# Kernel tuning notes

Measured on AMD Instinct MI355X. Metric: run time of the kernel, lower is better.

The kernel has to match this reference:

```python
import jax, jax.numpy as jnp
import numpy as np

MEM = 2048

def _linear_params(key, scale):
    kw, kb = jax.random.split(key)
    W = jax.random.uniform(kw, (MEM, MEM), jnp.float32, -scale, scale)
    b = jax.random.uniform(kb, (MEM,), jnp.float32, -scale, scale)
    return W, b

def setup_inputs() -> dict:
    key = jax.random.key(0)
    ks = jax.random.split(key, 18)
    scale = 1.0 / np.sqrt(MEM)
    inp = {
        'lc': jax.random.normal(ks[0], (1, MEM), jnp.float32),
        'lh': jax.random.normal(ks[1], (1, MEM), jnp.float32),
        'rc': jax.random.normal(ks[2], (1, MEM), jnp.float32),
        'rh': jax.random.normal(ks[3], (1, MEM), jnp.float32),
        'S': jax.random.normal(ks[4], (1, MEM), jnp.float32),
        'w': jax.random.normal(ks[5], (1, MEM), jnp.float32),
    }
    names = ['Wh', 'Us', 'ma', 'ilh', 'irh', 'lflh', 'lfrh', 'rflh', 'rfrh', 'ulh', 'urh']
    for i, n in enumerate(names):
        W, b = _linear_params(ks[6 + i], scale)
        inp[n + '_w'] = W
        inp[n + '_b'] = b
    return inp

def _lin(x, W, b):
    return x @ W.T + b

def reference(lc, lh, rc, rh, S, w,
              Wh_w, Wh_b, Us_w, Us_b, ma_w, ma_b,
              ilh_w, ilh_b, irh_w, irh_b,
              lflh_w, lflh_b, lfrh_w, lfrh_b,
              rflh_w, rflh_b, rfrh_w, rfrh_b,
              ulh_w, ulh_b, urh_w, urh_b):
    # attention scoring over the two children
    m_left = jnp.tanh(_lin(lh, Wh_w, Wh_b) + _lin(S, Us_w, Us_b)).squeeze()   # [MEM]
    m_right = jnp.tanh(_lin(rh, Wh_w, Wh_b) + _lin(S, Us_w, Us_b)).squeeze()  # [MEM]
    exp_left = w @ m_left[:, None]    # [1,1]
    exp_right = w @ m_right[:, None]  # [1,1]
    denom = exp_left + exp_right
    left_alpha = exp_left / denom
    right_alpha = exp_right / denom
    # attention-weighted child hidden states
    la = jnp.tanh(_lin(left_alpha * lh, ma_w, ma_b))   # [1,MEM]
    ra = jnp.tanh(_lin(right_alpha * rh, ma_w, ma_b))  # [1,MEM]
    # tree-LSTM gates
    i = jax.nn.sigmoid(_lin(la, ilh_w, ilh_b) + _lin(ra, irh_w, irh_b))
    lf = jax.nn.sigmoid(_lin(la, lflh_w, lflh_b) + _lin(ra, lfrh_w, lfrh_b))
    rf = jax.nn.sigmoid(_lin(la, rflh_w, rflh_b) + _lin(ra, rfrh_w, rfrh_b))
    update = jnp.tanh(_lin(la, ulh_w, ulh_b) + _lin(ra, urh_w, urh_b))
    c = i * update + lf * lc + rf * rc
    h = jnp.tanh(c)
    return (c, h)
```

## Files before the change

kernel.cpp:

```cpp
#include <hip/hip_runtime.h>
#include <hip/hip_bf16.h>
#include <math.h>

#define MEM 2048
#define NT  256
#define NF4 (MEM / 4)

__device__ __forceinline__ float dot4(float4 a, float4 b) {
    return a.x * b.x + a.y * b.y + a.z * b.z + a.w * b.w;
}

__device__ __forceinline__ float wave_reduce(float v) {
#pragma unroll
    for (int off = 32; off > 0; off >>= 1)
        v += __shfl_down(v, off, 64);
    return v;
}

__device__ __forceinline__ float sigmoidf_(float x) {
    return 1.0f / (1.0f + expf(-x));
}

__global__ __launch_bounds__(NT) void
k1_score(const float* __restrict__ lh, const float* __restrict__ rh,
         const float* __restrict__ S,  const float* __restrict__ w,
         const float* __restrict__ Wh_w, const float* __restrict__ Wh_b,
         const float* __restrict__ Us_w, const float* __restrict__ Us_b,
         const float* __restrict__ ma_w,
         float* __restrict__ pl, float* __restrict__ pr,
         float* __restrict__ wml, float* __restrict__ wmr)
{
    __shared__ float s_red[4][5];

    const int t   = threadIdx.x;
    const int row = blockIdx.x;

    const float4* __restrict__ wh4 = (const float4*)(Wh_w + (size_t)row * MEM);
    const float4* __restrict__ us4 = (const float4*)(Us_w + (size_t)row * MEM);
    const float4* __restrict__ ma4 = (const float4*)(ma_w + (size_t)row * MEM);
    const float4* __restrict__ l4  = (const float4*)lh;
    const float4* __restrict__ r4  = (const float4*)rh;
    const float4* __restrict__ s4  = (const float4*)S;

    float awl = 0.f, awr = 0.f, aus = 0.f, aml = 0.f, amr = 0.f;
#pragma unroll
    for (int h = 0; h < 2; ++h) {
        const int i = t + h * NT;
        const float4 a  = wh4[i];
        const float4 u  = us4[i];
        const float4 m  = ma4[i];
        const float4 xl = l4[i];
        const float4 xr = r4[i];
        const float4 xs = s4[i];
        awl += dot4(a, xl);
        awr += dot4(a, xr);
        aus += dot4(u, xs);
        aml += dot4(m, xl);
        amr += dot4(m, xr);
    }
    awl = wave_reduce(awl);
    awr = wave_reduce(awr);
    aus = wave_reduce(aus);
    aml = wave_reduce(aml);
    amr = wave_reduce(amr);

    const int wv = t >> 6, ln = t & 63;
    if (ln == 0) {
        s_red[wv][0] = awl; s_red[wv][1] = awr; s_red[wv][2] = aus;
        s_red[wv][3] = aml; s_red[wv][4] = amr;
    }
    __syncthreads();
    if (t == 0) {
        float r0 = 0.f, r1 = 0.f, r2 = 0.f, r3 = 0.f, r4v = 0.f;
#pragma unroll
        for (int k = 0; k < 4; ++k) {
            r0 += s_red[k][0]; r1 += s_red[k][1]; r2 += s_red[k][2];
            r3 += s_red[k][3]; r4v += s_red[k][4];
        }
        const float us = r2 + Us_b[row];
        const float ml = tanhf(r0 + Wh_b[row] + us);
        const float mr = tanhf(r1 + Wh_b[row] + us);
        pl[row] = r3;
        pr[row] = r4v;
        const float wj = w[row];
        wml[row] = wj * ml;
        wmr[row] = wj * mr;
    }
}

__global__ __launch_bounds__(NT) void
k2_gates(const float* __restrict__ lc, const float* __restrict__ rc,
         const float* __restrict__ pl, const float* __restrict__ pr,
         const float* __restrict__ wml, const float* __restrict__ wmr,
         const float* __restrict__ ma_b,
         const float* __restrict__ ilh_w,  const float* __restrict__ ilh_b,
         const float* __restrict__ irh_w,  const float* __restrict__ irh_b,
         const float* __restrict__ lflh_w, const float* __restrict__ lflh_b,
         const float* __restrict__ lfrh_w, const float* __restrict__ lfrh_b,
         const float* __restrict__ rflh_w, const float* __restrict__ rflh_b,
         const float* __restrict__ rfrh_w, const float* __restrict__ rfrh_b,
         const float* __restrict__ ulh_w,  const float* __restrict__ ulh_b,
         const float* __restrict__ urh_w,  const float* __restrict__ urh_b,
         float* __restrict__ out)
{
    __shared__ __align__(16) float s_la[MEM];
    __shared__ __align__(16) float s_ra[MEM];
    __shared__ float s_red[4][4];
    __shared__ float s_al[2];

    const int t   = threadIdx.x;
    const int wv  = t >> 6, ln = t & 63;
    const int row = blockIdx.x;

    {
        const float4* __restrict__ wl4 = (const float4*)wml;
        const float4* __restrict__ wr4 = (const float4*)wmr;
        const float4 a0 = wl4[t], a1 = wl4[t + NT];
        const float4 b0 = wr4[t], b1 = wr4[t + NT];
        float el = a0.x + a0.y + a0.z + a0.w + a1.x + a1.y + a1.z + a1.w;
        float er = b0.x + b0.y + b0.z + b0.w + b1.x + b1.y + b1.z + b1.w;
        el = wave_reduce(el);
        er = wave_reduce(er);
        if (ln == 0) { s_red[wv][0] = el; s_red[wv][1] = er; }
    }
    __syncthreads();
    if (t == 0) {
        const float el = s_red[0][0] + s_red[1][0] + s_red[2][0] + s_red[3][0];
        const float er = s_red[0][1] + s_red[1][1] + s_red[2][1] + s_red[3][1];
        const float d  = el + er;
        s_al[0] = el / d;
        s_al[1] = er / d;
    }
    __syncthreads();
    const float al = s_al[0];
    const float ar = s_al[1];

    {
        const float4* __restrict__ p4 = (const float4*)pl;
        const float4* __restrict__ q4 = (const float4*)pr;
        const float4* __restrict__ b4 = (const float4*)ma_b;
        float4* sla4 = (float4*)s_la;
        float4* sra4 = (float4*)s_ra;
#pragma unroll
        for (int h = 0; h < 2; ++h) {
            const int i = t + h * NT;
            const float4 p = p4[i];
            const float4 q = q4[i];
            const float4 b = b4[i];
            float4 la, ra;
            la.x = tanhf(al * p.x + b.x); ra.x = tanhf(ar * q.x + b.x);
            la.y = tanhf(al * p.y + b.y); ra.y = tanhf(ar * q.y + b.y);
            la.z = tanhf(al * p.z + b.z); ra.z = tanhf(ar * q.z + b.z);
            la.w = tanhf(al * p.w + b.w); ra.w = tanhf(ar * q.w + b.w);
            sla4[i] = la;
            sra4[i] = ra;
        }
    }
    __syncthreads();

    const size_t off = (size_t)row * MEM;
    const float4* __restrict__ il4  = (const float4*)(ilh_w  + off);
    const float4* __restrict__ ir4  = (const float4*)(irh_w  + off);
    const float4* __restrict__ lfl4 = (const float4*)(lflh_w + off);
    const float4* __restrict__ lfr4 = (const float4*)(lfrh_w + off);
    const float4* __restrict__ rfl4 = (const float4*)(rflh_w + off);
    const float4* __restrict__ rfr4 = (const float4*)(rfrh_w + off);
    const float4* __restrict__ ul4  = (const float4*)(ulh_w  + off);
    const float4* __restrict__ ur4  = (const float4*)(urh_w  + off);
    const float4* sla4 = (const float4*)s_la;
    const float4* sra4 = (const float4*)s_ra;

    float gi = 0.f, glf = 0.f, grf = 0.f, gu = 0.f;
#pragma unroll
    for (int h = 0; h < 2; ++h) {
        const int i = t + h * NT;
        const float4 w0 = il4[i];
        const float4 w1 = ir4[i];
        const float4 w2 = lfl4[i];
        const float4 w3 = lfr4[i];
        const float4 w4 = rfl4[i];
        const float4 w5 = rfr4[i];
        const float4 w6 = ul4[i];
        const float4 w7 = ur4[i];
        const float4 xa = sla4[i];
        const float4 xb = sra4[i];
        gi  += dot4(w0, xa) + dot4(w1, xb);
        glf += dot4(w2, xa) + dot4(w3, xb);
        grf += dot4(w4, xa) + dot4(w5, xb);
        gu  += dot4(w6, xa) + dot4(w7, xb);
    }
    gi  = wave_reduce(gi);
    glf = wave_reduce(glf);
    grf = wave_reduce(grf);
    gu  = wave_reduce(gu);
    if (ln == 0) {
        s_red[wv][0] = gi; s_red[wv][1] = glf; s_red[wv][2] = grf; s_red[wv][3] = gu;
    }
    __syncthreads();
    if (t == 0) {
        float r0 = 0.f, r1 = 0.f, r2 = 0.f, r3 = 0.f;
#pragma unroll
        for (int k = 0; k < 4; ++k) {
            r0 += s_red[k][0]; r1 += s_red[k][1];
            r2 += s_red[k][2]; r3 += s_red[k][3];
        }
        const float ig  = sigmoidf_(r0 + ilh_b[row]  + irh_b[row]);
        const float lfg = sigmoidf_(r1 + lflh_b[row] + lfrh_b[row]);
        const float rfg = sigmoidf_(r2 + rflh_b[row] + rfrh_b[row]);
        const float ug  = tanhf(r3 + ulh_b[row] + urh_b[row]);
        const float c   = ig * ug + lfg * lc[row] + rfg * rc[row];
        out[row]       = c;
        out[MEM + row] = tanhf(c);
    }
}

extern "C" void kernel_launch(void* const* d_in, const int* in_sizes, int n_in,
                              void* d_out, int out_size, void* d_ws, size_t ws_size,
                              hipStream_t stream) {
    const float* lc = (const float*)d_in[0];
    const float* lh = (const float*)d_in[1];
    const float* rc = (const float*)d_in[2];
    const float* rh = (const float*)d_in[3];
    const float* S  = (const float*)d_in[4];
    const float* w  = (const float*)d_in[5];
    const float* Wh_w   = (const float*)d_in[6];   const float* Wh_b   = (const float*)d_in[7];
    const float* Us_w   = (const float*)d_in[8];   const float* Us_b   = (const float*)d_in[9];
    const float* ma_w   = (const float*)d_in[10];  const float* ma_b   = (const float*)d_in[11];
    const float* ilh_w  = (const float*)d_in[12];  const float* ilh_b  = (const float*)d_in[13];
    const float* irh_w  = (const float*)d_in[14];  const float* irh_b  = (const float*)d_in[15];
    const float* lflh_w = (const float*)d_in[16];  const float* lflh_b = (const float*)d_in[17];
    const float* lfrh_w = (const float*)d_in[18];  const float* lfrh_b = (const float*)d_in[19];
    const float* rflh_w = (const float*)d_in[20];  const float* rflh_b = (const float*)d_in[21];
    const float* rfrh_w = (const float*)d_in[22];  const float* rfrh_b = (const float*)d_in[23];
    const float* ulh_w  = (const float*)d_in[24];  const float* ulh_b  = (const float*)d_in[25];
    const float* urh_w  = (const float*)d_in[26];  const float* urh_b  = (const float*)d_in[27];

    float* out = (float*)d_out;
    float* ws  = (float*)d_ws;
    float* pl  = ws;
    float* pr  = ws + MEM;
    float* wml = ws + 2 * MEM;
    float* wmr = ws + 3 * MEM;

    k1_score<<<MEM, NT, 0, stream>>>(lh, rh, S, w, Wh_w, Wh_b, Us_w, Us_b,
                                     ma_w, pl, pr, wml, wmr);

    k2_gates<<<MEM, NT, 0, stream>>>(lc, rc, pl, pr, wml, wmr, ma_b,
                                     ilh_w, ilh_b, irh_w, irh_b,
                                     lflh_w, lflh_b, lfrh_w, lfrh_b,
                                     rflh_w, rflh_b, rfrh_w, rfrh_b,
                                     ulh_w, ulh_b, urh_w, urh_b, out);
}
```

Measured before the change: 243.2 us.

## Process two output rows per block, keep activations in registers, use fast math

Both kernels now handle two weight rows per block, which halves the grid and reuses the loaded input vectors across both rows. In the gate kernel the attention activations stay in registers instead of going through shared memory, which removes the shared staging and one barrier. tanh and sigmoid use __expf-based fast approximations, and bias loads are hoisted to the start of the kernel. Each thread now issues more loads at once, which raises register pressure, and the fast math approximations may change numerical accuracy slightly.

```diff
diff --git a/kernel.cpp b/kernel.cpp
--- a/kernel.cpp
+++ b/kernel.cpp
@@ -1,10 +1,19 @@
 #include <hip/hip_runtime.h>
-#include <hip/hip_bf16.h>
 #include <math.h>
 
-#define MEM 2048
-#define NT  256
-#define NF4 (MEM / 4)
+#define MEM  2048
+#define NT   256
+#define NBLK (MEM / 2)
+
+struct Params {
+    const float *lc, *rc, *lh, *rh, *S, *w;
+    const float *Wh_w, *Wh_b, *Us_w, *Us_b, *ma_w, *ma_b;
+    const float *ilh_w, *ilh_b, *irh_w, *irh_b;
+    const float *lflh_w, *lflh_b, *lfrh_w, *lfrh_b;
+    const float *rflh_w, *rflh_b, *rfrh_w, *rfrh_b;
+    const float *ulh_w, *ulh_b, *urh_w, *urh_b;
+    float *pl, *pr, *wml, *wmr, *out;
+};
 
 __device__ __forceinline__ float dot4(float4 a, float4 b) {
     return a.x * b.x + a.y * b.y + a.z * b.z + a.w * b.w;
@@ -17,104 +26,123 @@
     return v;
 }
 
-__device__ __forceinline__ float sigmoidf_(float x) {
-    return 1.0f / (1.0f + expf(-x));
-}
-
-__global__ __launch_bounds__(NT) void
-k1_score(const float* __restrict__ lh, const float* __restrict__ rh,
-         const float* __restrict__ S,  const float* __restrict__ w,
-         const float* __restrict__ Wh_w, const float* __restrict__ Wh_b,
-         const float* __restrict__ Us_w, const float* __restrict__ Us_b,
-         const float* __restrict__ ma_w,
-         float* __restrict__ pl, float* __restrict__ pr,
-         float* __restrict__ wml, float* __restrict__ wmr)
+__device__ __forceinline__ float tanh_fast(float x) {
+    x = fminf(15.0f, fmaxf(-15.0f, x));
+    const float e = __expf(2.0f * x);
+    return (e - 1.0f) / (e + 1.0f);
+}
+__device__ __forceinline__ float sigmoid_fast(float x) {
+    return 1.0f / (1.0f + __expf(-x));
+}
+
+__global__ __launch_bounds__(NT, 4) void k1(Params p)
 {
-    __shared__ float s_red[4][5];
-
-    const int t   = threadIdx.x;
-    const int row = blockIdx.x;
-
-    const float4* __restrict__ wh4 = (const float4*)(Wh_w + (size_t)row * MEM);
-    const float4* __restrict__ us4 = (const float4*)(Us_w + (size_t)row * MEM);
-    const float4* __restrict__ ma4 = (const float4*)(ma_w + (size_t)row * MEM);
-    const float4* __restrict__ l4  = (const float4*)lh;
-    const float4* __restrict__ r4  = (const float4*)rh;
-    const float4* __restrict__ s4  = (const float4*)S;
-
-    float awl = 0.f, awr = 0.f, aus = 0.f, aml = 0.f, amr = 0.f;
+    __shared__ float s_red[4][10];
+
+    const int t  = threadIdx.x;
+    const int wv = t >> 6, ln = t & 63;
+    const int r0 = (int)blockIdx.x * 2;
+    const int r1 = r0 + 1;
+
+    const float whb0 = p.Wh_b[r0], whb1 = p.Wh_b[r1];
+    const float usb0 = p.Us_b[r0], usb1 = p.Us_b[r1];
+    const float w0s  = p.w[r0],    w1s  = p.w[r1];
+
+    const float4* l4 = (const float4*)p.lh;
+    const float4* r4 = (const float4*)p.rh;
+    const float4* s4 = (const float4*)p.S;
+    const float4 xl[2] = { l4[t], l4[t + NT] };
+    const float4 xr[2] = { r4[t], r4[t + NT] };
+    const float4 xs[2] = { s4[t], s4[t + NT] };
+
+    const float4* wh0 = (const float4*)(p.Wh_w + (size_t)r0 * MEM);
+    const float4* wh1 = (const float4*)(p.Wh_w + (size_t)r1 * MEM);
+    const float4* us0 = (const float4*)(p.Us_w + (size_t)r0 * MEM);
+    const float4* us1 = (const float4*)(p.Us_w + (size_t)r1 * MEM);
+    const float4* ma0 = (const float4*)(p.ma_w + (size_t)r0 * MEM);
+    const float4* ma1 = (const float4*)(p.ma_w + (size_t)r1 * MEM);
+
+    float awl0 = 0.f, awr0 = 0.f, aus0 = 0.f, aml0 = 0.f, amr0 = 0.f;
+    float awl1 = 0.f, awr1 = 0.f, aus1 = 0.f, aml1 = 0.f, amr1 = 0.f;
 #pragma unroll
     for (int h = 0; h < 2; ++h) {
         const int i = t + h * NT;
-        const float4 a  = wh4[i];
-        const float4 u  = us4[i];
-        const float4 m  = ma4[i];
-        const float4 xl = l4[i];
-        const float4 xr = r4[i];
-        const float4 xs = s4[i];
-        awl += dot4(a, xl);
-        awr += dot4(a, xr);
-        aus += dot4(u, xs);
-        aml += dot4(m, xl);
-        amr += dot4(m, xr);
-    }
-    awl = wave_reduce(awl);
-    awr = wave_reduce(awr);
-    aus = wave_reduce(aus);
-    aml = wave_reduce(aml);
-    amr = wave_reduce(amr);
-
-    const int wv = t >> 6, ln = t & 63;
+        const float4 a0 = wh0[i];
+        const float4 a1 = wh1[i];
+        const float4 u0 = us0[i];
+        const float4 u1 = us1[i];
+        const float4 m0 = ma0[i];
+        const float4 m1 = ma1[i];
+        awl0 += dot4(a0, xl[h]);  awl1 += dot4(a1, xl[h]);
+        awr0 += dot4(a0, xr[h]);  awr1 += dot4(a1, xr[h]);
+        aus0 += dot4(u0, xs[h]);  aus1 += dot4(u1, xs[h]);
+        aml0 += dot4(m0, xl[h]);  aml1 += dot4(m1, xl[h]);
+        amr0 += dot4(m0, xr[h]);  amr1 += dot4(m1, xr[h]);
+    }
+    awl0 = wave_reduce(awl0);  awl1 = wave_reduce(awl1);
+    awr0 = wave_reduce(awr0);  awr1 = wave_reduce(awr1);
+    aus0 = wave_reduce(aus0);  aus1 = wave_reduce(aus1);
+    aml0 = wave_reduce(aml0);  aml1 = wave_reduce(aml1);
+    amr0 = wave_reduce(amr0);  amr1 = wave_reduce(amr1);
+
     if (ln == 0) {
-        s_red[wv][0] = awl; s_red[wv][1] = awr; s_red[wv][2] = aus;
-        s_red[wv][3] = aml; s_red[wv][4] = amr;
+        s_red[wv][0] = awl0; s_red[wv][1] = awr0; s_red[wv][2] = aus0;
+        s_red[wv][3] = aml0; s_red[wv][4] = amr0;
+        s_red[wv][5] = awl1; s_red[wv][6] = awr1; s_red[wv][7] = aus1;
+        s_red[wv][8] = aml1; s_red[wv][9] = amr1;
     }
     __syncthreads();
     if (t == 0) {
-        float r0 = 0.f, r1 = 0.f, r2 = 0.f, r3 = 0.f, r4v = 0.f;
-#pragma unroll
-        for (int k = 0; k < 4; ++k) {
-            r0 += s_red[k][0]; r1 += s_red[k][1]; r2 += s_red[k][2];
-            r3 += s_red[k][3]; r4v += s_red[k][4];
+        const float whbv[2] = { whb0, whb1 };
+        const float usbv[2] = { usb0, usb1 };
+        const float wsv[2]  = { w0s, w1s };
+#pragma unroll
+        for (int rr = 0; rr < 2; ++rr) {
+            float v0 = 0.f, v1 = 0.f, v2 = 0.f, v3 = 0.f, v4 = 0.f;
+#pragma unroll
+            for (int k = 0; k < 4; ++k) {
+                v0 += s_red[k][rr * 5 + 0];
+                v1 += s_red[k][rr * 5 + 1];
+                v2 += s_red[k][rr * 5 + 2];
+                v3 += s_red[k][rr * 5 + 3];
+                v4 += s_red[k][rr * 5 + 4];
+            }
+            const float usx = v2 + usbv[rr];
+            const float ml = tanh_fast(v0 + whbv[rr] + usx);
+            const float mr = tanh_fast(v1 + whbv[rr] + usx);
+            const int row = r0 + rr;
+            p.pl[row]  = v3;
+            p.pr[row]  = v4;
+            p.wml[row] = wsv[rr] * ml;
+            p.wmr[row] = wsv[rr] * mr;
         }
-        const float us = r2 + Us_b[row];
-        const float ml = tanhf(r0 + Wh_b[row] + us);
-        const float mr = tanhf(r1 + Wh_b[row] + us);
-        pl[row] = r3;
-        pr[row] = r4v;
-        const float wj = w[row];
-        wml[row] = wj * ml;
-        wmr[row] = wj * mr;
-    }
-}
-
-__global__ __launch_bounds__(NT) void
-k2_gates(const float* __restrict__ lc, const float* __restrict__ rc,
-         const float* __restrict__ pl, const float* __restrict__ pr,
-         const float* __restrict__ wml, const float* __restrict__ wmr,
-         const float* __restrict__ ma_b,
-         const float* __restrict__ ilh_w,  const float* __restrict__ ilh_b,
-         const float* __restrict__ irh_w,  const float* __restrict__ irh_b,
-         const float* __restrict__ lflh_w, const float* __restrict__ lflh_b,
-         const float* __restrict__ lfrh_w, const float* __restrict__ lfrh_b,
-         const float* __restrict__ rflh_w, const float* __restrict__ rflh_b,
-         const float* __restrict__ rfrh_w, const float* __restrict__ rfrh_b,
-         const float* __restrict__ ulh_w,  const float* __restrict__ ulh_b,
-         const float* __restrict__ urh_w,  const float* __restrict__ urh_b,
-         float* __restrict__ out)
+    }
+}
+
+__global__ __launch_bounds__(NT, 4) void k2(Params p)
 {
-    __shared__ __align__(16) float s_la[MEM];
-    __shared__ __align__(16) float s_ra[MEM];
-    __shared__ float s_red[4][4];
+    __shared__ float s_red[4][8];
     __shared__ float s_al[2];
 
-    const int t   = threadIdx.x;
-    const int wv  = t >> 6, ln = t & 63;
-    const int row = blockIdx.x;
+    const int t  = threadIdx.x;
+    const int wv = t >> 6, ln = t & 63;
+    const int r0 = (int)blockIdx.x * 2;
+    const int r1 = r0 + 1;
+
+    const float bI0  = p.ilh_b[r0]  + p.irh_b[r0];
+    const float bI1  = p.ilh_b[r1]  + p.irh_b[r1];
+    const float bLF0 = p.lflh_b[r0] + p.lfrh_b[r0];
+    const float bLF1 = p.lflh_b[r1] + p.lfrh_b[r1];
+    const float bRF0 = p.rflh_b[r0] + p.rfrh_b[r0];
+    const float bRF1 = p.rflh_b[r1] + p.rfrh_b[r1];
+    const float bU0  = p.ulh_b[r0]  + p.urh_b[r0];
+    const float bU1  = p.ulh_b[r1]  + p.urh_b[r1];
+    const float lc0  = p.lc[r0], lc1 = p.lc[r1];
+    const float rc0  = p.rc[r0], rc1 = p.rc[r1];
 
     {
-        const float4* __restrict__ wl4 = (const float4*)wml;
-        const float4* __restrict__ wr4 = (const float4*)wmr;
+        const float4* wl4 = (const float4*)p.wml;
+        const float4* wr4 = (const float4*)p.wmr;
         const float4 a0 = wl4[t], a1 = wl4[t + NT];
         const float4 b0 = wr4[t], b1 = wr4[t + NT];
         float el = a0.x + a0.y + a0.z + a0.w + a1.x + a1.y + a1.z + a1.w;
@@ -135,119 +163,144 @@
     const float al = s_al[0];
     const float ar = s_al[1];
 
+    float4 xa[2], xb[2];
     {
-        const float4* __restrict__ p4 = (const float4*)pl;
-        const float4* __restrict__ q4 = (const float4*)pr;
-        const float4* __restrict__ b4 = (const float4*)ma_b;
-        float4* sla4 = (float4*)s_la;
-        float4* sra4 = (float4*)s_ra;
+        const float4* p4 = (const float4*)p.pl;
+        const float4* q4 = (const float4*)p.pr;
+        const float4* b4 = (const float4*)p.ma_b;
 #pragma unroll
         for (int h = 0; h < 2; ++h) {
             const int i = t + h * NT;
-            const float4 p = p4[i];
-            const float4 q = q4[i];
-            const float4 b = b4[i];
-            float4 la, ra;
-            la.x = tanhf(al * p.x + b.x); ra.x = tanhf(ar * q.x + b.x);
-            la.y = tanhf(al * p.y + b.y); ra.y = tanhf(ar * q.y + b.y);
-            la.z = tanhf(al * p.z + b.z); ra.z = tanhf(ar * q.z + b.z);
-            la.w = tanhf(al * p.w + b.w); ra.w = tanhf(ar * q.w + b.w);
-            sla4[i] = la;
-            sra4[i] = ra;
+            const float4 pp = p4[i];
+            const float4 qq = q4[i];
+            const float4 bb = b4[i];
+            xa[h].x = tanh_fast(al * pp.x + bb.x); xb[h].x = tanh_fast(ar * qq.x + bb.x);
+            xa[h].y = tanh_fast(al * pp.y + bb.y); xb[h].y = tanh_fast(ar * qq.y + bb.y);
+            xa[h].z = tanh_fast(al * pp.z + bb.z); xb[h].z = tanh_fast(ar * qq.z + bb.z);
+            xa[h].w = tanh_fast(al * pp.w + bb.w); xb[h].w = tanh_fast(ar * qq.w + bb.w);
         }
     }
-    __syncthreads();
-
-    const size_t off = (size_t)row * MEM;
-    const float4* __restrict__ il4  = (const float4*)(ilh_w  + off);
-    const float4* __restrict__ ir4  = (const float4*)(irh_w  + off);
-    const float4* __restrict__ lfl4 = (const float4*)(lflh_w + off);
-    const float4* __restrict__ lfr4 = (const float4*)(lfrh_w + off);
-    const float4* __restrict__ rfl4 = (const float4*)(rflh_w + off);
-    const float4* __restrict__ rfr4 = (const float4*)(rfrh_w + off);
-    const float4* __restrict__ ul4  = (const float4*)(ulh_w  + off);
-    const float4* __restrict__ ur4  = (const float4*)(urh_w  + off);
-    const float4* sla4 = (const float4*)s_la;
-    const float4* sra4 = (const float4*)s_ra;
-
-    float gi = 0.f, glf = 0.f, grf = 0.f, gu = 0.f;
+
+    const size_t o0 = (size_t)r0 * MEM;
+    const size_t o1 = (size_t)r1 * MEM;
+    const float4* il4_0  = (const float4*)(p.ilh_w  + o0);
+    const float4* il4_1  = (const float4*)(p.ilh_w  + o1);
+    const float4* ir4_0  = (const float4*)(p.irh_w  + o0);
+    const float4* ir4_1  = (const float4*)(p.irh_w  + o1);
+    const float4* lfl4_0 = (const float4*)(p.lflh_w + o0);
+    const float4* lfl4_1 = (const float4*)(p.lflh_w + o1);
+    const float4* lfr4_0 = (const float4*)(p.lfrh_w + o0);
+    const float4* lfr4_1 = (const float4*)(p.lfrh_w + o1);
+    const float4* rfl4_0 = (const float4*)(p.rflh_w + o0);
+    const float4* rfl4_1 = (const float4*)(p.rflh_w + o1);
+    const float4* rfr4_0 = (const float4*)(p.rfrh_w + o0);
+    const float4* rfr4_1 = (const float4*)(p.rfrh_w + o1);
+    const float4* ul4_0  = (const float4*)(p.ulh_w  + o0);
+    const float4* ul4_1  = (const float4*)(p.ulh_w  + o1);
+    const float4* ur4_0  = (const float4*)(p.urh_w  + o0);
+    const float4* ur4_1  = (const float4*)(p.urh_w  + o1);
+
+    float gi0 = 0.f, glf0 = 0.f, grf0 = 0.f, gu0 = 0.f;
+    float gi1 = 0.f, glf1 = 0.f, grf1 = 0.f, gu1 = 0.f;
 #pragma unroll
     for (int h = 0; h < 2; ++h) {
         const int i = t + h * NT;
-        const float4 w0 = il4[i];
-        const float4 w1 = ir4[i];
-        const float4 w2 = lfl4[i];
-        const float4 w3 = lfr4[i];
-        const float4 w4 = rfl4[i];
-        const float4 w5 = rfr4[i];
-        const float4 w6 = ul4[i];
-        const float4 w7 = ur4[i];
-        const float4 xa = sla4[i];
-        const float4 xb = sra4[i];
-        gi  += dot4(w0, xa) + dot4(w1, xb);
-        glf += dot4(w2, xa) + dot4(w3, xb);
-        grf += dot4(w4, xa) + dot4(w5, xb);
-        gu  += dot4(w6, xa) + dot4(w7, xb);
-    }
-    gi  = wave_reduce(gi);
-    glf = wave_reduce(glf);
-    grf = wave_reduce(grf);
-    gu  = wave_reduce(gu);
+        const float4 wA = il4_0[i];
+        const float4 wB = ir4_0[i];
+        const float4 wC = lfl4_0[i];
+        const float4 wD = lfr4_0[i];
+        const float4 wE = rfl4_0[i];
+        const float4 wF = rfr4_0[i];
+        const float4 wG = ul4_0[i];
+        const float4 wH = ur4_0[i];
+        const float4 wI = il4_1[i];
+        const float4 wJ = ir4_1[i];
+        const float4 wK = lfl4_1[i];
+        const float4 wL = lfr4_1[i];
+        const float4 wM = rfl4_1[i];
+        const float4 wN = rfr4_1[i];
+        const float4 wO = ul4_1[i];
+        const float4 wP = ur4_1[i];
+        gi0  += dot4(wA, xa[h]) + dot4(wB, xb[h]);
+        glf0 += dot4(wC, xa[h]) + dot4(wD, xb[h]);
+        grf0 += dot4(wE, xa[h]) + dot4(wF, xb[h]);
+        gu0  += dot4(wG, xa[h]) + dot4(wH, xb[h]);
+        gi1  += dot4(wI, xa[h]) + dot4(wJ, xb[h]);
+        glf1 += dot4(wK, xa[h]) + dot4(wL, xb[h]);
+        grf1 += dot4(wM, xa[h]) + dot4(wN, xb[h]);
+        gu1  += dot4(wO, xa[h]) + dot4(wP, xb[h]);
+    }
+    gi0  = wave_reduce(gi0);   gi1  = wave_reduce(gi1);
+    glf0 = wave_reduce(glf0);  glf1 = wave_reduce(glf1);
+    grf0 = wave_reduce(grf0);  grf1 = wave_reduce(grf1);
+    gu0  = wave_reduce(gu0);   gu1  = wave_reduce(gu1);
+
     if (ln == 0) {
-        s_red[wv][0] = gi; s_red[wv][1] = glf; s_red[wv][2] = grf; s_red[wv][3] = gu;
+        s_red[wv][0] = gi0;  s_red[wv][1] = glf0;
+        s_red[wv][2] = grf0; s_red[wv][3] = gu0;
+        s_red[wv][4] = gi1;  s_red[wv][5] = glf1;
+        s_red[wv][6] = grf1; s_red[wv][7] = gu1;
     }
     __syncthreads();
     if (t == 0) {
-        float r0 = 0.f, r1 = 0.f, r2 = 0.f, r3 = 0.f;
-#pragma unroll
-        for (int k = 0; k < 4; ++k) {
-            r0 += s_red[k][0]; r1 += s_red[k][1];
-            r2 += s_red[k][2]; r3 += s_red[k][3];
+        const float bIv[2]  = { bI0, bI1 };
+        const float bLFv[2] = { bLF0, bLF1 };
+        const float bRFv[2] = { bRF0, bRF1 };
+        const float bUv[2]  = { bU0, bU1 };
+        const float lcv[2]  = { lc0, lc1 };
+        const float rcv[2]  = { rc0, rc1 };
+#pragma unroll
+        for (int rr = 0; rr < 2; ++rr) {
+            float g0 = 0.f, g1 = 0.f, g2 = 0.f, g3 = 0.f;
+#pragma unroll
+            for (int k = 0; k < 4; ++k) {
+                g0 += s_red[k][rr * 4 + 0];
+                g1 += s_red[k][rr * 4 + 1];
+                g2 += s_red[k][rr * 4 + 2];
+                g3 += s_red[k][rr * 4 + 3];
+            }
+            const float ig  = sigmoid_fast(g0 + bIv[rr]);
+            const float lfg = sigmoid_fast(g1 + bLFv[rr]);
+            const float rfg = sigmoid_fast(g2 + bRFv[rr]);
+            const float ug  = tanh_fast(g3 + bUv[rr]);
+            const float c   = ig * ug + lfg * lcv[rr] + rfg * rcv[rr];
+            const int row = r0 + rr;
+            p.out[row]       = c;
+            p.out[MEM + row] = tanh_fast(c);
         }
-        const float ig  = sigmoidf_(r0 + ilh_b[row]  + irh_b[row]);
-        const float lfg = sigmoidf_(r1 + lflh_b[row] + lfrh_b[row]);
-        const float rfg = sigmoidf_(r2 + rflh_b[row] + rfrh_b[row]);
-        const float ug  = tanhf(r3 + ulh_b[row] + urh_b[row]);
-        const float c   = ig * ug + lfg * lc[row] + rfg * rc[row];
-        out[row]       = c;
-        out[MEM + row] = tanhf(c);
     }
 }
 
 extern "C" void kernel_launch(void* const* d_in, const int* in_sizes, int n_in,
                               void* d_out, int out_size, void* d_ws, size_t ws_size,
-                              hipStream_t stream) {
-    const float* lc = (const float*)d_in[0];
-    const float* lh = (const float*)d_in[1];
-    const float* rc = (const float*)d_in[2];
-    const float* rh = (const float*)d_in[3];
-    const float* S  = (const float*)d_in[4];
-    const float* w  = (const float*)d_in[5];
-    const float* Wh_w   = (const float*)d_in[6];   const float* Wh_b   = (const float*)d_in[7];
-    const float* Us_w   = (const float*)d_in[8];   const float* Us_b   = (const float*)d_in[9];
-    const float* ma_w   = (const float*)d_in[10];  const float* ma_b   = (const float*)d_in[11];
-    const float* ilh_w  = (const float*)d_in[12];  const float* ilh_b  = (const float*)d_in[13];
-    const float* irh_w  = (const float*)d_in[14];  const float* irh_b  = (const float*)d_in[15];
-    const float* lflh_w = (const float*)d_in[16];  const float* lflh_b = (const float*)d_in[17];
-    const float* lfrh_w = (const float*)d_in[18];  const float* lfrh_b = (const float*)d_in[19];
-    const float* rflh_w = (const float*)d_in[20];  const float* rflh_b = (const float*)d_in[21];
-    const float* rfrh_w = (const float*)d_in[22];  const float* rfrh_b = (const float*)d_in[23];
-    const float* ulh_w  = (const float*)d_in[24];  const float* ulh_b  = (const float*)d_in[25];
-    const float* urh_w  = (const float*)d_in[26];  const float* urh_b  = (const float*)d_in[27];
-
-    float* out = (float*)d_out;
-    float* ws  = (float*)d_ws;
-    float* pl  = ws;
-    float* pr  = ws + MEM;
-    float* wml = ws + 2 * MEM;
-    float* wmr = ws + 3 * MEM;
-
-    k1_score<<<MEM, NT, 0, stream>>>(lh, rh, S, w, Wh_w, Wh_b, Us_w, Us_b,
-                                     ma_w, pl, pr, wml, wmr);
-
-    k2_gates<<<MEM, NT, 0, stream>>>(lc, rc, pl, pr, wml, wmr, ma_b,
-                                     ilh_w, ilh_b, irh_w, irh_b,
-                                     lflh_w, lflh_b, lfrh_w, lfrh_b,
-                                     rflh_w, rflh_b, rfrh_w, rfrh_b,
-                                     ulh_w, ulh_b, urh_w, urh_b, out);
-}
+                              hipStream_t stream)
+{
+    Params h;
+    h.lc = (const float*)d_in[0];
+    h.lh = (const float*)d_in[1];
+    h.rc = (const float*)d_in[2];
+    h.rh = (const float*)d_in[3];
+    h.S  = (const float*)d_in[4];
+    h.w  = (const float*)d_in[5];
+    h.Wh_w   = (const float*)d_in[6];   h.Wh_b   = (const float*)d_in[7];
+    h.Us_w   = (const float*)d_in[8];   h.Us_b   = (const float*)d_in[9];
+    h.ma_w   = (const float*)d_in[10];  h.ma_b   = (const float*)d_in[11];
+    h.ilh_w  = (const float*)d_in[12];  h.ilh_b  = (const float*)d_in[13];
+    h.irh_w  = (const float*)d_in[14];  h.irh_b  = (const float*)d_in[15];
+    h.lflh_w = (const float*)d_in[16];  h.lflh_b = (const float*)d_in[17];
+    h.lfrh_w = (const float*)d_in[18];  h.lfrh_b = (const float*)d_in[19];
+    h.rflh_w = (const float*)d_in[20];  h.rflh_b = (const float*)d_in[21];
+    h.rfrh_w = (const float*)d_in[22];  h.rfrh_b = (const float*)d_in[23];
+    h.ulh_w  = (const float*)d_in[24];  h.ulh_b  = (const float*)d_in[25];
+    h.urh_w  = (const float*)d_in[26];  h.urh_b  = (const float*)d_in[27];
+
+    float* ws = (float*)d_ws;
+    h.pl  = ws;
+    h.pr  = ws + MEM;
+    h.wml = ws + 2 * MEM;
+    h.wmr = ws + 3 * MEM;
+    h.out = (float*)d_out;
+
+    k1<<<NBLK, NT, 0, stream>>>(h);
+    k2<<<NBLK, NT, 0, stream>>>(h);
+}
```

After: 247.9 us. No clear change (+1.9%).
